# Kernel optimization log

Measured on AMD Instinct MI355X. Metric: run time of the kernel, lower is better.

The kernel has to match this reference:

```python
import jax, jax.numpy as jnp
import numpy as np

D_MODEL = 1024
NUM_HEADS = 16
HEAD_DIM = D_MODEL // NUM_HEADS


def setup_inputs() -> dict:
    key = jax.random.key(0)
    ks = jax.random.split(key, 9)
    s = D_MODEL ** -0.5  # roughly like nn.Linear init scale
    x = jax.random.normal(ks[0], (4, 2048, D_MODEL), dtype=jnp.float32)
    Wq = jax.random.normal(ks[1], (D_MODEL, D_MODEL), dtype=jnp.float32) * s
    bq = jax.random.normal(ks[2], (D_MODEL,), dtype=jnp.float32) * s
    Wk = jax.random.normal(ks[3], (D_MODEL, D_MODEL), dtype=jnp.float32) * s
    bk = jax.random.normal(ks[4], (D_MODEL,), dtype=jnp.float32) * s
    Wv = jax.random.normal(ks[5], (D_MODEL, D_MODEL), dtype=jnp.float32) * s
    bv = jax.random.normal(ks[6], (D_MODEL,), dtype=jnp.float32) * s
    Wo = jax.random.normal(ks[7], (D_MODEL, D_MODEL), dtype=jnp.float32) * s
    bo = jax.random.normal(ks[8], (D_MODEL,), dtype=jnp.float32) * s
    return {"x": x, "Wq": Wq, "bq": bq, "Wk": Wk, "bk": bk,
            "Wv": Wv, "bv": bv, "Wo": Wo, "bo": bo}


def reference(x, Wq, bq, Wk, bk, Wv, bv, Wo, bo):
    B, S, D = x.shape
    H, Dh = NUM_HEADS, HEAD_DIM
    scale = Dh ** -0.5
    # nn.Linear: x @ W.T + b
    q = (x @ Wq.T + bq).reshape(B, S, H, Dh)
    k = (x @ Wk.T + bk).reshape(B, S, H, Dh)
    v = (x @ Wv.T + bv).reshape(B, S, H, Dh)
    # scores: (B, H, S, S), full materialization as in the original bmm path
    dp = scale * jnp.einsum('bqhd,bkhd->bhqk', q, k)
    att = jax.nn.softmax(dp, axis=-1)
    out = jnp.einsum('bhqk,bkhd->bqhd', att, v).reshape(B, S, D)
    return out @ Wo.T + bo
```

## Files before the change

kernel.cpp:

```cpp
#include <hip/hip_runtime.h>
#include <stdint.h>

typedef __attribute__((ext_vector_type(8))) __bf16 bf16x8;
typedef __attribute__((ext_vector_type(4))) float floatx4;

#define DEV __device__ __forceinline__

DEV unsigned short f2bf(float f) {
    union { float f; unsigned u; } uf; uf.f = f;
    unsigned u = uf.u;
    unsigned r = (u + 0x7fffu + ((u >> 16) & 1u)) >> 16;
    return (unsigned short)r;
}

DEV float fast_exp2(float x) {
#if __has_builtin(__builtin_amdgcn_exp2f)
    return __builtin_amdgcn_exp2f(x);
#else
    return exp2f(x);
#endif
}

DEV unsigned pack_trunc2(float lo, float hi) {
    return __builtin_amdgcn_perm(__float_as_uint(hi), __float_as_uint(lo), 0x07060302u);
}

DEV void async16(const void* g, void* l) {
    __builtin_amdgcn_global_load_lds(
        (const __attribute__((address_space(1))) void*)g,
        (__attribute__((address_space(3))) void*)l, 16, 0, 0);
}

__global__ void cast_all_kernel(const float* __restrict__ x,
                                const float* __restrict__ Wq, const float* __restrict__ Wk,
                                const float* __restrict__ Wv, const float* __restrict__ Wo,
                                const float* __restrict__ bq, const float* __restrict__ bk,
                                const float* __restrict__ bv,
                                unsigned short* __restrict__ xb,
                                unsigned short* __restrict__ wqkv,
                                unsigned short* __restrict__ wo,
                                float* __restrict__ bqkv) {
    const int NX = 2097152;
    const int NW = 262144;
    int i = blockIdx.x * blockDim.x + threadIdx.x;
    if (i < NX) {
        float4 v = reinterpret_cast<const float4*>(x)[i];
        ushort4 o;
        o.x = f2bf(v.x); o.y = f2bf(v.y); o.z = f2bf(v.z); o.w = f2bf(v.w);
        reinterpret_cast<ushort4*>(xb)[i] = o;
        return;
    }
    int j = i - NX;
    if (j < 4 * NW) {
        int seg = j >> 18, off = j & (NW - 1);
        const float* src = (seg == 0) ? Wq : (seg == 1) ? Wk : (seg == 2) ? Wv : Wo;
        unsigned short* dst = (seg < 3) ? (wqkv + seg * 1048576) : wo;
        float4 v = reinterpret_cast<const float4*>(src)[off];
        ushort4 o;
        o.x = f2bf(v.x); o.y = f2bf(v.y); o.z = f2bf(v.z); o.w = f2bf(v.w);
        reinterpret_cast<ushort4*>(dst)[off] = o;
        return;
    }
    int k = j - 4 * NW;
    if (k < 768) {
        int seg = k >> 8, off = k & 255;
        const float* src = (seg == 0) ? bq : (seg == 1) ? bk : bv;
        reinterpret_cast<float4*>(bqkv)[k] = reinterpret_cast<const float4*>(src)[off];
    }
}

template <int MODE>
__global__ __launch_bounds__(256)
void gemm128(const unsigned short* __restrict__ A,
             const unsigned short* __restrict__ B,
             const float* __restrict__ bias,
             unsigned short* __restrict__ q_ws,
             unsigned short* __restrict__ k_ws,
             unsigned short* __restrict__ v_ws,
             float* __restrict__ fout) {
    constexpr int K = 1024;
    __shared__ alignas(16) unsigned short smem[128 * 136];
    unsigned short* sA = smem;
    unsigned short* sB = smem + 128 * 64;
    unsigned short* sT = smem;
    float* sT32 = reinterpret_cast<float*>(smem);

    const int tid = threadIdx.x;
    const int w = tid >> 6, lane = tid & 63, quad = lane >> 4, l16 = lane & 15;
    const int wr = w >> 1, wc = w & 1;
    const int bm = blockIdx.x, bn = blockIdx.y;
    const int arow0 = bm * 128, brow0 = bn * 128;

    floatx4 acc[4][4];
#pragma unroll
    for (int i = 0; i < 4; i++)
#pragma unroll
        for (int j = 0; j < 4; j++) acc[i][j] = (floatx4){0.f, 0.f, 0.f, 0.f};

    for (int k0 = 0; k0 < K; k0 += 64) {
#pragma unroll
        for (int i = 0; i < 4; i++) {
            int cb = i * 256 + w * 64;
            int ci = cb + lane;
            int row = ci >> 3, cl = ci & 7, cs = cl ^ (row & 7);
            async16(A + (size_t)(arow0 + row) * K + k0 + cs * 8, (char*)sA + cb * 16);
            async16(B + (size_t)(brow0 + row) * K + k0 + cs * 8, (char*)sB + cb * 16);
        }
        __syncthreads();
#pragma unroll
        for (int kk = 0; kk < 2; kk++) {
            bf16x8 aF[4], bF[4];
#pragma unroll
            for (int i = 0; i < 4; i++) {
                int row = wr * 64 + i * 16 + l16;
                int c = kk * 4 + quad, ph = c ^ (row & 7);
                aF[i] = *reinterpret_cast<const bf16x8*>(sA + row * 64 + ph * 8);
            }
#pragma unroll
            for (int j = 0; j < 4; j++) {
                int row = wc * 64 + j * 16 + l16;
                int c = kk * 4 + quad, ph = c ^ (row & 7);
                bF[j] = *reinterpret_cast<const bf16x8*>(sB + row * 64 + ph * 8);
            }
#pragma unroll
            for (int i = 0; i < 4; i++)
#pragma unroll
                for (int j = 0; j < 4; j++)
                    acc[i][j] = __builtin_amdgcn_mfma_f32_16x16x32_bf16(
                        aF[i], bF[j], acc[i][j], 0, 0, 0);
        }
        __syncthreads();
    }

    if (MODE == 1) {
#pragma unroll
        for (int ch = 0; ch < 2; ch++) {
            if (ch) __syncthreads();
            if (wr == ch) {
#pragma unroll
                for (int j = 0; j < 4; j++) {
                    const int c = wc * 64 + j * 16 + l16;
                    const float bia = bias[brow0 + c];
#pragma unroll
                    for (int i = 0; i < 4; i++) {
                        int s_loc = i * 16 + quad * 4;
#pragma unroll
                        for (int r = 0; r < 4; r++)
                            sT32[(s_loc + r) * 132 + c] = acc[i][j][r] + bia;
                    }
                }
            }
            __syncthreads();
            const int cpos = (tid & 31) * 4;
#pragma unroll
            for (int it = 0; it < 8; it++) {
                int s_loc = (tid >> 5) + it * 8;
                int grow = arow0 + ch * 64 + s_loc;
                float4 vv = *reinterpret_cast<const float4*>(sT32 + s_loc * 132 + cpos);
                *reinterpret_cast<float4*>(fout + (size_t)grow * 1024 + brow0 + cpos) = vv;
            }
        }
    } else if (bn < 16) {
        unsigned short* dst = (bn < 8) ? q_ws : k_ws;
        const float sc = (bn < 8) ? 0.18033688f : 1.0f;
#pragma unroll
        for (int j = 0; j < 4; j++) {
            const int c = wc * 64 + j * 16 + l16;
            const float bia = bias[brow0 + c];
#pragma unroll
            for (int i = 0; i < 4; i++) {
                int s_loc = wr * 64 + i * 16 + quad * 4;
#pragma unroll
                for (int r = 0; r < 4; r++)
                    sT[(s_loc + r) * 136 + c] = f2bf((acc[i][j][r] + bia) * sc);
            }
        }
        __syncthreads();
        const int nnbase = (bn & 7) * 128;
        const int c0 = (tid & 15) * 8;
        const int h = (nnbase + c0) >> 6, d = c0 & 63;
#pragma unroll
        for (int it = 0; it < 8; it++) {
            int s_loc = (tid >> 4) + it * 16;
            int s = arow0 + s_loc;
            int bb = s >> 11, s4 = s & 2047;
            uint4 vdat = *reinterpret_cast<const uint4*>(sT + s_loc * 136 + c0);
            *reinterpret_cast<uint4*>(
                dst + ((size_t)(bb * 16 + h) * 2048 + s4) * 64 + d) = vdat;
        }
    } else {
#pragma unroll
        for (int j = 0; j < 4; j++) {
            const int c = wc * 64 + j * 16 + l16;
            const float bia = bias[brow0 + c];
#pragma unroll
            for (int i = 0; i < 4; i++) {
#pragma unroll
                for (int r = 0; r < 4; r++) {
                    int v = wr * 64 + (quad * 4 + r) * 4 + i;
                    sT[c * 136 + v] = f2bf(acc[i][j][r] + bia);
                }
            }
        }
        __syncthreads();
        const int bb = bm >> 4, blk = bm & 15;
        const int chunk = tid & 15;
#pragma unroll
        for (int it = 0; it < 8; it++) {
            int row = (tid >> 4) + it * 16;
            int h = (bn - 16) * 2 + (row >> 6), d = row & 63;
            ushort4 lo = *reinterpret_cast<const ushort4*>(sT + row * 136 + chunk * 8);
            ushort4 hi = *reinterpret_cast<const ushort4*>(sT + row * 136 + chunk * 8 + 4);
            size_t off = ((size_t)(bb * 16 + h) * 64 + d) * 2048 + blk * 128 + chunk * 8;
            *reinterpret_cast<ushort4*>(v_ws + off) = lo;
            *reinterpret_cast<ushort4*>(v_ws + off + 4) = hi;
        }
    }
}

__global__ __launch_bounds__(256, 4)
void attn_kernel(const unsigned short* __restrict__ q_ws,
                 const unsigned short* __restrict__ k_ws,
                 const unsigned short* __restrict__ v_ws,
                 unsigned short* __restrict__ o_ws) {
    __shared__ alignas(16) unsigned short smem[20480];

    const int tid = threadIdx.x;
    const int w = tid >> 6, lane = tid & 63, quad = lane >> 4, l16 = lane & 15;
    const int id = blockIdx.x;
    const int bh = (id >> 8) * 8 + (id & 7);
    const int q0 = ((id >> 3) & 31) * 64;
    const size_t base = (size_t)bh * 2048 * 64;

    unsigned short* sPw = smem + 16384 + w * 1024;

    bf16x8 aQ[2];
    {
        int qrow = q0 + w * 16 + l16;
        const unsigned short* qp = q_ws + base + (size_t)qrow * 64 + quad * 8;
        aQ[0] = *reinterpret_cast<const bf16x8*>(qp);
        aQ[1] = *reinterpret_cast<const bf16x8*>(qp + 32);
    }

    const unsigned short* kg[2];
    const unsigned short* vg[2];
    int loff[2];
#pragma unroll
    for (int it = 0; it < 2; it++) {
        int ci = it * 256 + tid;
        int row = ci >> 3, cl = ci & 7, cs = cl ^ (row & 7);
        kg[it] = k_ws + base + (size_t)row * 64 + cs * 8;
        vg[it] = v_ws + base + (size_t)row * 2048 + cs * 8;
        loff[it] = ci * 8;
    }

    const __bf16 one = (__bf16)1.0f;
    const bf16x8 vOnes = {one, one, one, one, one, one, one, one};

    floatx4 oAcc[4], rsAcc;
#pragma unroll
    for (int j = 0; j < 4; j++) oAcc[j] = (floatx4){0.f, 0.f, 0.f, 0.f};
    rsAcc = (floatx4){0.f, 0.f, 0.f, 0.f};

    {
#pragma unroll
        for (int it = 0; it < 2; it++) {
            async16(kg[it], smem + loff[it]);
            async16(vg[it], smem + 8192 + loff[it]);
        }
    }

    for (int t = 0; t < 32; t++) {
        const int b = t & 1;
        const unsigned short* sK = smem + b * 4096;
        const unsigned short* sVt = smem + 8192 + b * 4096;
        __syncthreads();

        if (t < 31) {
            const int kv0 = (t + 1) * 64;
            unsigned short* dK = smem + (b ^ 1) * 4096;
            unsigned short* dV = smem + 8192 + (b ^ 1) * 4096;
#pragma unroll
            for (int it = 0; it < 2; it++) {
                async16(kg[it] + (size_t)kv0 * 64, dK + loff[it]);
                async16(vg[it] + kv0, dV + loff[it]);
            }
        }

        floatx4 sAcc[4];
#pragma unroll
        for (int j = 0; j < 4; j++) sAcc[j] = (floatx4){0.f, 0.f, 0.f, 0.f};
#pragma unroll
        for (int kk = 0; kk < 2; kk++) {
#pragma unroll
            for (int j = 0; j < 4; j++) {
                int krow = j * 16 + l16;
                int ph = (kk * 4 + quad) ^ (krow & 7);
                bf16x8 aK = *reinterpret_cast<const bf16x8*>(sK + krow * 64 + ph * 8);
                sAcc[j] = __builtin_amdgcn_mfma_f32_16x16x32_bf16(aK, aQ[kk], sAcc[j], 0, 0, 0);
            }
        }

        {
            float e00 = fast_exp2(sAcc[0][0]), e10 = fast_exp2(sAcc[1][0]);
            float e20 = fast_exp2(sAcc[2][0]), e30 = fast_exp2(sAcc[3][0]);
            float e01 = fast_exp2(sAcc[0][1]), e11 = fast_exp2(sAcc[1][1]);
            float e21 = fast_exp2(sAcc[2][1]), e31 = fast_exp2(sAcc[3][1]);
            float e02 = fast_exp2(sAcc[0][2]), e12 = fast_exp2(sAcc[1][2]);
            float e22 = fast_exp2(sAcc[2][2]), e32 = fast_exp2(sAcc[3][2]);
            float e03 = fast_exp2(sAcc[0][3]), e13 = fast_exp2(sAcc[1][3]);
            float e23 = fast_exp2(sAcc[2][3]), e33 = fast_exp2(sAcc[3][3]);
            uint4 w0, w1;
            w0.x = pack_trunc2(e00, e10);
            w0.y = pack_trunc2(e20, e30);
            w0.z = pack_trunc2(e01, e11);
            w0.w = pack_trunc2(e21, e31);
            w1.x = pack_trunc2(e02, e12);
            w1.y = pack_trunc2(e22, e32);
            w1.z = pack_trunc2(e03, e13);
            w1.w = pack_trunc2(e23, e33);
            const int xr = l16 & 7;
            *reinterpret_cast<uint4*>(sPw + l16 * 64 + (((2 * quad) ^ xr) << 3)) = w0;
            *reinterpret_cast<uint4*>(sPw + l16 * 64 + (((2 * quad + 1) ^ xr) << 3)) = w1;
        }
        asm volatile("s_waitcnt lgkmcnt(0)" ::: "memory");
        __builtin_amdgcn_sched_barrier(0);

        bf16x8 aP[2];
#pragma unroll
        for (int ks = 0; ks < 2; ks++)
            aP[ks] = *reinterpret_cast<const bf16x8*>(
                sPw + l16 * 64 + (((ks * 4 + quad) ^ (l16 & 7)) << 3));
#pragma unroll
        for (int jd = 0; jd < 4; jd++) {
            int drow = jd * 16 + l16;
#pragma unroll
            for (int ks = 0; ks < 2; ks++) {
                int ph = (ks * 4 + quad) ^ (drow & 7);
                bf16x8 bV = *reinterpret_cast<const bf16x8*>(sVt + drow * 64 + ph * 8);
                oAcc[jd] = __builtin_amdgcn_mfma_f32_16x16x32_bf16(aP[ks], bV, oAcc[jd], 0, 0, 0);
            }
        }
#pragma unroll
        for (int ks = 0; ks < 2; ks++)
            rsAcc = __builtin_amdgcn_mfma_f32_16x16x32_bf16(aP[ks], vOnes, rsAcc, 0, 0, 0);
    }

    float inv[4];
#pragma unroll
    for (int r = 0; r < 4; r++) inv[r] = 1.0f / rsAcc[r];
    const int bb = bh >> 4, h = bh & 15;
#pragma unroll
    for (int jd = 0; jd < 4; jd++) {
        int d = jd * 16 + l16;
#pragma unroll
        for (int r = 0; r < 4; r++) {
            int s = q0 + w * 16 + quad * 4 + r;
            float v = oAcc[jd][r] * inv[r];
            o_ws[((size_t)bb * 2048 + s) * 1024 + h * 64 + d] = f2bf(v);
        }
    }
}

extern "C" void kernel_launch(void* const* d_in, const int* in_sizes, int n_in,
                              void* d_out, int out_size, void* d_ws, size_t ws_size,
                              hipStream_t stream) {
    const float* x  = (const float*)d_in[0];
    const float* Wq = (const float*)d_in[1];
    const float* bq = (const float*)d_in[2];
    const float* Wk = (const float*)d_in[3];
    const float* bk = (const float*)d_in[4];
    const float* Wv = (const float*)d_in[5];
    const float* bv = (const float*)d_in[6];
    const float* Wo = (const float*)d_in[7];
    const float* bo = (const float*)d_in[8];
    float* out = (float*)d_out;

    char* ws = (char*)d_ws;
    unsigned short* xb   = (unsigned short*)(ws);
    unsigned short* wqkv = (unsigned short*)(ws + (16ull << 20));
    unsigned short* wo   = (unsigned short*)(ws + (22ull << 20));
    float*          bqkv = (float*)(ws + (24ull << 20));
    unsigned short* q_ws = (unsigned short*)(ws + (25ull << 20));
    unsigned short* k_ws = (unsigned short*)(ws + (41ull << 20));
    unsigned short* v_ws = (unsigned short*)(ws + (57ull << 20));
    unsigned short* o_ws = xb;

    cast_all_kernel<<<12291, 256, 0, stream>>>(x, Wq, Wk, Wv, Wo, bq, bk, bv,
                                               xb, wqkv, wo, bqkv);

    gemm128<0><<<dim3(64, 24), 256, 0, stream>>>(xb, wqkv, bqkv, q_ws, k_ws, v_ws, nullptr);
    attn_kernel<<<2048, 256, 0, stream>>>(q_ws, k_ws, v_ws, o_ws);
    gemm128<1><<<dim3(64, 8), 256, 0, stream>>>(o_ws, wo, bo, nullptr, nullptr, nullptr, out);
}
```

Measured before the change: 281.0 us.

## Load V fragments directly from global into registers, shrink LDS, raise occupancy

The attention kernel no longer stages V tiles through double-buffered LDS with async copies. Each wave instead loads its own transposed-V fragments straight from global memory into registers at the start of every KV step. This frees 16KB of LDS, and the launch bound goes from 4 to 6 blocks per CU. The goal is to cut LDS traffic and raise occupancy. In exchange, each wave does redundant global/L2 reads of V with no prefetch, and the load latency is only hidden behind the QK MFMAs and softmax.

```diff
diff --git a/kernel.cpp b/kernel.cpp
--- a/kernel.cpp
+++ b/kernel.cpp
@@ -218,12 +218,12 @@
     }
 }
 
-__global__ __launch_bounds__(256, 4)
+__global__ __launch_bounds__(256, 6)
 void attn_kernel(const unsigned short* __restrict__ q_ws,
                  const unsigned short* __restrict__ k_ws,
                  const unsigned short* __restrict__ v_ws,
                  unsigned short* __restrict__ o_ws) {
-    __shared__ alignas(16) unsigned short smem[20480];
+    __shared__ alignas(16) unsigned short smem[12288];
 
     const int tid = threadIdx.x;
     const int w = tid >> 6, lane = tid & 63, quad = lane >> 4, l16 = lane & 15;
@@ -232,7 +232,7 @@
     const int q0 = ((id >> 3) & 31) * 64;
     const size_t base = (size_t)bh * 2048 * 64;
 
-    unsigned short* sPw = smem + 16384 + w * 1024;
+    unsigned short* sPw = smem + 8192 + w * 1024;
 
     bf16x8 aQ[2];
     {
@@ -243,16 +243,15 @@
     }
 
     const unsigned short* kg[2];
-    const unsigned short* vg[2];
     int loff[2];
 #pragma unroll
     for (int it = 0; it < 2; it++) {
         int ci = it * 256 + tid;
         int row = ci >> 3, cl = ci & 7, cs = cl ^ (row & 7);
         kg[it] = k_ws + base + (size_t)row * 64 + cs * 8;
-        vg[it] = v_ws + base + (size_t)row * 2048 + cs * 8;
         loff[it] = ci * 8;
     }
+    const unsigned short* vbase = v_ws + base + (size_t)l16 * 2048 + quad * 8;
 
     const __bf16 one = (__bf16)1.0f;
     const bf16x8 vOnes = {one, one, one, one, one, one, one, one};
@@ -264,28 +263,29 @@
 
     {
 #pragma unroll
-        for (int it = 0; it < 2; it++) {
-            async16(kg[it], smem + loff[it]);
-            async16(vg[it], smem + 8192 + loff[it]);
-        }
+        for (int it = 0; it < 2; it++) async16(kg[it], smem + loff[it]);
     }
 
     for (int t = 0; t < 32; t++) {
         const int b = t & 1;
         const unsigned short* sK = smem + b * 4096;
-        const unsigned short* sVt = smem + 8192 + b * 4096;
         __syncthreads();
 
         if (t < 31) {
             const int kv0 = (t + 1) * 64;
             unsigned short* dK = smem + (b ^ 1) * 4096;
-            unsigned short* dV = smem + 8192 + (b ^ 1) * 4096;
-#pragma unroll
-            for (int it = 0; it < 2; it++) {
+#pragma unroll
+            for (int it = 0; it < 2; it++)
                 async16(kg[it] + (size_t)kv0 * 64, dK + loff[it]);
-                async16(vg[it] + kv0, dV + loff[it]);
-            }
-        }
+        }
+
+        bf16x8 bV[4][2];
+#pragma unroll
+        for (int jd = 0; jd < 4; jd++)
+#pragma unroll
+            for (int ks = 0; ks < 2; ks++)
+                bV[jd][ks] = *reinterpret_cast<const bf16x8*>(
+                    vbase + (size_t)(jd * 16) * 2048 + t * 64 + ks * 32);
 
         floatx4 sAcc[4];
 #pragma unroll
@@ -333,13 +333,10 @@
                 sPw + l16 * 64 + (((ks * 4 + quad) ^ (l16 & 7)) << 3));
 #pragma unroll
         for (int jd = 0; jd < 4; jd++) {
-            int drow = jd * 16 + l16;
-#pragma unroll
-            for (int ks = 0; ks < 2; ks++) {
-                int ph = (ks * 4 + quad) ^ (drow & 7);
-                bf16x8 bV = *reinterpret_cast<const bf16x8*>(sVt + drow * 64 + ph * 8);
-                oAcc[jd] = __builtin_amdgcn_mfma_f32_16x16x32_bf16(aP[ks], bV, oAcc[jd], 0, 0, 0);
-            }
+#pragma unroll
+            for (int ks = 0; ks < 2; ks++)
+                oAcc[jd] = __builtin_amdgcn_mfma_f32_16x16x32_bf16(
+                    aP[ks], bV[jd][ks], oAcc[jd], 0, 0, 0);
         }
 #pragma unroll
         for (int ks = 0; ks < 2; ks++)
```

After: 630.0 us. 124% more time.

## Process two 64-row query groups per attention block to reuse K/V tiles

Applied to the files above, without the earlier changes.

Each attention block now handles 128 query rows (two groups of 64) instead of 64, so every K/V tile loaded into shared memory is used by twice as many queries. The grid is halved to 1024 blocks. This halves global K/V traffic and the async-copy and barrier overhead per query. In exchange each thread holds more registers (double the accumulators and Q fragments), and with fewer blocks the GPU may have less occupancy and less parallelism.

```diff
diff --git a/kernel.cpp b/kernel.cpp
--- a/kernel.cpp
+++ b/kernel.cpp
@@ -228,18 +228,19 @@
     const int tid = threadIdx.x;
     const int w = tid >> 6, lane = tid & 63, quad = lane >> 4, l16 = lane & 15;
     const int id = blockIdx.x;
-    const int bh = (id >> 8) * 8 + (id & 7);
-    const int q0 = ((id >> 3) & 31) * 64;
+    const int bh = (id >> 7) * 8 + (id & 7);
+    const int q0 = ((id >> 3) & 15) * 128;
     const size_t base = (size_t)bh * 2048 * 64;
 
     unsigned short* sPw = smem + 16384 + w * 1024;
 
-    bf16x8 aQ[2];
-    {
-        int qrow = q0 + w * 16 + l16;
+    bf16x8 aQ[2][2];
+#pragma unroll
+    for (int g = 0; g < 2; g++) {
+        int qrow = q0 + g * 64 + w * 16 + l16;
         const unsigned short* qp = q_ws + base + (size_t)qrow * 64 + quad * 8;
-        aQ[0] = *reinterpret_cast<const bf16x8*>(qp);
-        aQ[1] = *reinterpret_cast<const bf16x8*>(qp + 32);
+        aQ[g][0] = *reinterpret_cast<const bf16x8*>(qp);
+        aQ[g][1] = *reinterpret_cast<const bf16x8*>(qp + 32);
     }
 
     const unsigned short* kg[2];
@@ -257,10 +258,13 @@
     const __bf16 one = (__bf16)1.0f;
     const bf16x8 vOnes = {one, one, one, one, one, one, one, one};
 
-    floatx4 oAcc[4], rsAcc;
-#pragma unroll
-    for (int j = 0; j < 4; j++) oAcc[j] = (floatx4){0.f, 0.f, 0.f, 0.f};
-    rsAcc = (floatx4){0.f, 0.f, 0.f, 0.f};
+    floatx4 oAcc[2][4], rsAcc[2];
+#pragma unroll
+    for (int g = 0; g < 2; g++) {
+#pragma unroll
+        for (int j = 0; j < 4; j++) oAcc[g][j] = (floatx4){0.f, 0.f, 0.f, 0.f};
+        rsAcc[g] = (floatx4){0.f, 0.f, 0.f, 0.f};
+    }
 
     {
 #pragma unroll
@@ -287,77 +291,86 @@
             }
         }
 
-        floatx4 sAcc[4];
-#pragma unroll
-        for (int j = 0; j < 4; j++) sAcc[j] = (floatx4){0.f, 0.f, 0.f, 0.f};
-#pragma unroll
-        for (int kk = 0; kk < 2; kk++) {
-#pragma unroll
-            for (int j = 0; j < 4; j++) {
-                int krow = j * 16 + l16;
-                int ph = (kk * 4 + quad) ^ (krow & 7);
-                bf16x8 aK = *reinterpret_cast<const bf16x8*>(sK + krow * 64 + ph * 8);
-                sAcc[j] = __builtin_amdgcn_mfma_f32_16x16x32_bf16(aK, aQ[kk], sAcc[j], 0, 0, 0);
-            }
-        }
-
-        {
-            float e00 = fast_exp2(sAcc[0][0]), e10 = fast_exp2(sAcc[1][0]);
-            float e20 = fast_exp2(sAcc[2][0]), e30 = fast_exp2(sAcc[3][0]);
-            float e01 = fast_exp2(sAcc[0][1]), e11 = fast_exp2(sAcc[1][1]);
-            float e21 = fast_exp2(sAcc[2][1]), e31 = fast_exp2(sAcc[3][1]);
-            float e02 = fast_exp2(sAcc[0][2]), e12 = fast_exp2(sAcc[1][2]);
-            float e22 = fast_exp2(sAcc[2][2]), e32 = fast_exp2(sAcc[3][2]);
-            float e03 = fast_exp2(sAcc[0][3]), e13 = fast_exp2(sAcc[1][3]);
-            float e23 = fast_exp2(sAcc[2][3]), e33 = fast_exp2(sAcc[3][3]);
-            uint4 w0, w1;
-            w0.x = pack_trunc2(e00, e10);
-            w0.y = pack_trunc2(e20, e30);
-            w0.z = pack_trunc2(e01, e11);
-            w0.w = pack_trunc2(e21, e31);
-            w1.x = pack_trunc2(e02, e12);
-            w1.y = pack_trunc2(e22, e32);
-            w1.z = pack_trunc2(e03, e13);
-            w1.w = pack_trunc2(e23, e33);
-            const int xr = l16 & 7;
-            *reinterpret_cast<uint4*>(sPw + l16 * 64 + (((2 * quad) ^ xr) << 3)) = w0;
-            *reinterpret_cast<uint4*>(sPw + l16 * 64 + (((2 * quad + 1) ^ xr) << 3)) = w1;
-        }
-        asm volatile("s_waitcnt lgkmcnt(0)" ::: "memory");
-        __builtin_amdgcn_sched_barrier(0);
-
-        bf16x8 aP[2];
-#pragma unroll
-        for (int ks = 0; ks < 2; ks++)
-            aP[ks] = *reinterpret_cast<const bf16x8*>(
-                sPw + l16 * 64 + (((ks * 4 + quad) ^ (l16 & 7)) << 3));
+#pragma unroll
+        for (int g = 0; g < 2; g++) {
+            floatx4 sAcc[4];
+#pragma unroll
+            for (int j = 0; j < 4; j++) sAcc[j] = (floatx4){0.f, 0.f, 0.f, 0.f};
+#pragma unroll
+            for (int kk = 0; kk < 2; kk++) {
+#pragma unroll
+                for (int j = 0; j < 4; j++) {
+                    int krow = j * 16 + l16;
+                    int ph = (kk * 4 + quad) ^ (krow & 7);
+                    bf16x8 aK = *reinterpret_cast<const bf16x8*>(sK + krow * 64 + ph * 8);
+                    sAcc[j] = __builtin_amdgcn_mfma_f32_16x16x32_bf16(
+                        aK, aQ[g][kk], sAcc[j], 0, 0, 0);
+                }
+            }
+
+            {
+                float e00 = fast_exp2(sAcc[0][0]), e10 = fast_exp2(sAcc[1][0]);
+                float e20 = fast_exp2(sAcc[2][0]), e30 = fast_exp2(sAcc[3][0]);
+                float e01 = fast_exp2(sAcc[0][1]), e11 = fast_exp2(sAcc[1][1]);
+                float e21 = fast_exp2(sAcc[2][1]), e31 = fast_exp2(sAcc[3][1]);
+                float e02 = fast_exp2(sAcc[0][2]), e12 = fast_exp2(sAcc[1][2]);
+                float e22 = fast_exp2(sAcc[2][2]), e32 = fast_exp2(sAcc[3][2]);
+                float e03 = fast_exp2(sAcc[0][3]), e13 = fast_exp2(sAcc[1][3]);
+                float e23 = fast_exp2(sAcc[2][3]), e33 = fast_exp2(sAcc[3][3]);
+                uint4 w0, w1;
+                w0.x = pack_trunc2(e00, e10);
+                w0.y = pack_trunc2(e20, e30);
+                w0.z = pack_trunc2(e01, e11);
+                w0.w = pack_trunc2(e21, e31);
+                w1.x = pack_trunc2(e02, e12);
+                w1.y = pack_trunc2(e22, e32);
+                w1.z = pack_trunc2(e03, e13);
+                w1.w = pack_trunc2(e23, e33);
+                const int xr = l16 & 7;
+                *reinterpret_cast<uint4*>(sPw + l16 * 64 + (((2 * quad) ^ xr) << 3)) = w0;
+                *reinterpret_cast<uint4*>(sPw + l16 * 64 + (((2 * quad + 1) ^ xr) << 3)) = w1;
+            }
+            asm volatile("s_waitcnt lgkmcnt(0)" ::: "memory");
+            __builtin_amdgcn_sched_barrier(0);
+
+            bf16x8 aP[2];
+#pragma unroll
+            for (int ks = 0; ks < 2; ks++)
+                aP[ks] = *reinterpret_cast<const bf16x8*>(
+                    sPw + l16 * 64 + (((ks * 4 + quad) ^ (l16 & 7)) << 3));
+#pragma unroll
+            for (int jd = 0; jd < 4; jd++) {
+                int drow = jd * 16 + l16;
+#pragma unroll
+                for (int ks = 0; ks < 2; ks++) {
+                    int ph = (ks * 4 + quad) ^ (drow & 7);
+                    bf16x8 bV = *reinterpret_cast<const bf16x8*>(sVt + drow * 64 + ph * 8);
+                    oAcc[g][jd] = __builtin_amdgcn_mfma_f32_16x16x32_bf16(
+                        aP[ks], bV, oAcc[g][jd], 0, 0, 0);
+                }
+            }
+#pragma unroll
+            for (int ks = 0; ks < 2; ks++)
+                rsAcc[g] = __builtin_amdgcn_mfma_f32_16x16x32_bf16(
+                    aP[ks], vOnes, rsAcc[g], 0, 0, 0);
+        }
+    }
+
+    const int bb = bh >> 4, h = bh & 15;
+#pragma unroll
+    for (int g = 0; g < 2; g++) {
+        float inv[4];
+#pragma unroll
+        for (int r = 0; r < 4; r++) inv[r] = 1.0f / rsAcc[g][r];
 #pragma unroll
         for (int jd = 0; jd < 4; jd++) {
-            int drow = jd * 16 + l16;
-#pragma unroll
-            for (int ks = 0; ks < 2; ks++) {
-                int ph = (ks * 4 + quad) ^ (drow & 7);
-                bf16x8 bV = *reinterpret_cast<const bf16x8*>(sVt + drow * 64 + ph * 8);
-                oAcc[jd] = __builtin_amdgcn_mfma_f32_16x16x32_bf16(aP[ks], bV, oAcc[jd], 0, 0, 0);
-            }
-        }
-#pragma unroll
-        for (int ks = 0; ks < 2; ks++)
-            rsAcc = __builtin_amdgcn_mfma_f32_16x16x32_bf16(aP[ks], vOnes, rsAcc, 0, 0, 0);
-    }
-
-    float inv[4];
-#pragma unroll
-    for (int r = 0; r < 4; r++) inv[r] = 1.0f / rsAcc[r];
-    const int bb = bh >> 4, h = bh & 15;
-#pragma unroll
-    for (int jd = 0; jd < 4; jd++) {
-        int d = jd * 16 + l16;
-#pragma unroll
-        for (int r = 0; r < 4; r++) {
-            int s = q0 + w * 16 + quad * 4 + r;
-            float v = oAcc[jd][r] * inv[r];
-            o_ws[((size_t)bb * 2048 + s) * 1024 + h * 64 + d] = f2bf(v);
+            int d = jd * 16 + l16;
+#pragma unroll
+            for (int r = 0; r < 4; r++) {
+                int s = q0 + g * 64 + w * 16 + quad * 4 + r;
+                float v = oAcc[g][jd][r] * inv[r];
+                o_ws[((size_t)bb * 2048 + s) * 1024 + h * 64 + d] = f2bf(v);
+            }
         }
     }
 }
@@ -390,6 +403,6 @@
                                                xb, wqkv, wo, bqkv);
 
     gemm128<0><<<dim3(64, 24), 256, 0, stream>>>(xb, wqkv, bqkv, q_ws, k_ws, v_ws, nullptr);
-    attn_kernel<<<2048, 256, 0, stream>>>(q_ws, k_ws, v_ws, o_ws);
+    attn_kernel<<<1024, 256, 0, stream>>>(q_ws, k_ws, v_ws, o_ws);
     gemm128<1><<<dim3(64, 8), 256, 0, stream>>>(o_ws, wo, bo, nullptr, nullptr, nullptr, out);
 }
```

Result: no change. 275.9 us (-1.8%).
